# Kernel tuning notes

Hardware: AMD Instinct MI355X
Metric: run time of the kernel (lower is better)

Reference implementation:

```python
import jax, jax.numpy as jnp
import numpy as np

N_NODES = 50000
NEG_SLOPE = 0.2  # PyG GATConv default leaky_relu slope


def setup_inputs() -> dict:
    key = jax.random.key(0)
    ks = jax.random.split(key, 12)
    N, E, D_IN, H = N_NODES, 1200000, 128, 64
    sd_in = 1.0 / np.sqrt(D_IN)
    sd_h = 1.0 / np.sqrt(H)
    return {
        "x": jax.random.normal(ks[0], (N, D_IN), jnp.float32),
        "src": jax.random.randint(ks[1], (E,), 0, N, jnp.int32),
        "dst": jax.random.randint(ks[2], (E,), 0, N, jnp.int32),
        "W1_src": jax.random.normal(ks[3], (D_IN, H), jnp.float32) * sd_in,
        "W1_dst": jax.random.normal(ks[4], (D_IN, H), jnp.float32) * sd_in,
        "a1_src": jax.random.normal(ks[5], (H,), jnp.float32) * sd_h,
        "a1_dst": jax.random.normal(ks[6], (H,), jnp.float32) * sd_h,
        "b1": jnp.zeros((H,), jnp.float32),
        "W2_src": jax.random.normal(ks[7], (H, H), jnp.float32) * sd_h,
        "W2_dst": jax.random.normal(ks[8], (H, H), jnp.float32) * sd_h,
        "a2_src": jax.random.normal(ks[9], (H,), jnp.float32) * sd_h,
        "a2_dst": jax.random.normal(ks[10], (H,), jnp.float32) * sd_h,
        "b2": jnp.zeros((H,), jnp.float32),
    }


def _gat_layer(x, src, dst, W_src, W_dst, att_src, att_dst, bias):
    N = x.shape[0]
    h_src = x @ W_src            # [N, H] transformed source features
    h_dst = x @ W_dst            # [N, H] transformed destination features
    alpha_src = h_src @ att_src  # [N]
    alpha_dst = h_dst @ att_dst  # [N]
    # edge-wise attention logits (gather), edge j -> i: e = lrelu(a_src[j] + a_dst[i])
    e = jax.nn.leaky_relu(alpha_src[src] + alpha_dst[dst], NEG_SLOPE)  # [E]
    # segment softmax over incoming edges of each destination node
    m = jax.ops.segment_max(e, dst, num_segments=N)          # [N]
    ex = jnp.exp(e - m[dst])                                  # [E]
    denom = jax.ops.segment_sum(ex, dst, num_segments=N)     # [N]
    alpha = ex / denom[dst]                                   # [E]
    # weighted scatter-add aggregation
    msgs = h_src[src] * alpha[:, None]                        # [E, H]
    out = jax.ops.segment_sum(msgs, dst, num_segments=N)     # [N, H]
    return out + bias


def reference(x, src, dst, W1_src, W1_dst, a1_src, a1_dst, b1,
              W2_src, W2_dst, a2_src, a2_dst, b2):
    h = jnp.tanh(_gat_layer(x, src, dst, W1_src, W1_dst, a1_src, a1_dst, b1))
    h = jnp.tanh(_gat_layer(h, src, dst, W2_src, W2_dst, a2_src, a2_dst, b2))
    return h
```

## Files before the change

kernel.cpp:

```cpp
#include <hip/hip_runtime.h>
#include <hip/hip_bf16.h>

#define NEG_SLOPE 0.2f
#define EPB 4096

typedef __attribute__((ext_vector_type(8))) short short8v;
typedef __attribute__((ext_vector_type(4))) float f32x4;

__device__ inline float blo(unsigned u) { return __uint_as_float(u << 16); }
__device__ inline float bhi(unsigned u) { return __uint_as_float(u & 0xffff0000u); }
__device__ inline unsigned short bf16bits(float f) {
    __hip_bfloat16 b = __float2bfloat16(f);
    return *(unsigned short*)&b;
}
__device__ inline unsigned pack2bf(float e, float o) {
    return ((unsigned)bf16bits(o) << 16) | (unsigned)bf16bits(e);
}

__global__ void init_counts(int* __restrict__ bucket_cnt) {
    bucket_cnt[threadIdx.x] = 0;
}

__global__ __launch_bounds__(256) void bucket_hist(const int* __restrict__ dst,
                                                   int* __restrict__ bucket_cnt, int E) {
    __shared__ int lh[256];
    int tid = threadIdx.x;
    lh[tid] = 0;
    __syncthreads();
    for (int e = blockIdx.x * 256 + tid; e < E; e += gridDim.x * 256)
        atomicAdd(&lh[dst[e] >> 8], 1);
    __syncthreads();
    if (lh[tid]) atomicAdd(&bucket_cnt[tid], lh[tid]);
}

__global__ __launch_bounds__(256) void bucket_scan(const int* __restrict__ bucket_cnt,
                                                   int* __restrict__ bucket_base,
                                                   int* __restrict__ bucket_cursor, int NB) {
    __shared__ int tmp[256];
    int tid = threadIdx.x;
    int v = (tid < NB) ? bucket_cnt[tid] : 0;
    tmp[tid] = v;
    __syncthreads();
    for (int off = 1; off < 256; off <<= 1) {
        int t = (tid >= off) ? tmp[tid - off] : 0;
        __syncthreads();
        tmp[tid] += t;
        __syncthreads();
    }
    int excl = tmp[tid] - v;
    bucket_base[tid] = excl;
    bucket_cursor[tid] = excl;
    if (tid == 255) bucket_base[256] = tmp[255];
}

__global__ __launch_bounds__(256) void bucket_scatter(const int* __restrict__ src,
                                                      const int* __restrict__ dst,
                                                      int* __restrict__ bucket_cursor,
                                                      unsigned* __restrict__ ebuf, int E) {
    __shared__ int lhist[256];
    __shared__ int lbase[256];
    int tid = threadIdx.x;
    lhist[tid] = 0;
    __syncthreads();
    int base = blockIdx.x * EPB;
    int bkt[16], rank[16];
    unsigned pack[16];
    #pragma unroll
    for (int i = 0; i < 16; ++i) {
        int e = base + i * 256 + tid;
        bkt[i] = -1;
        if (e < E) {
            int d = dst[e], s = src[e];
            bkt[i]  = d >> 8;
            pack[i] = ((unsigned)(d & 255) << 16) | (unsigned)s;
            rank[i] = atomicAdd(&lhist[bkt[i]], 1);
        }
    }
    __syncthreads();
    int cnt = lhist[tid];
    if (cnt) lbase[tid] = atomicAdd(&bucket_cursor[tid], cnt);
    __syncthreads();
    #pragma unroll
    for (int i = 0; i < 16; ++i)
        if (bkt[i] >= 0) ebuf[lbase[bkt[i]] + rank[i]] = pack[i];
}

__global__ __launch_bounds__(256) void bucket_build(const unsigned* __restrict__ ebuf,
                                                    const int* __restrict__ bucket_base,
                                                    int* __restrict__ row_ptr,
                                                    int* __restrict__ csr_src,
                                                    int N, int E) {
    __shared__ int deg[256];
    __shared__ int cur[256];
    __shared__ int tmp[256];
    int b = blockIdx.x, tid = threadIdx.x;
    int ebase = bucket_base[b], eend = bucket_base[b + 1];
    deg[tid] = 0;
    __syncthreads();
    for (int e = ebase + tid; e < eend; e += 256)
        atomicAdd(&deg[ebuf[e] >> 16], 1);
    __syncthreads();
    int v = deg[tid];
    tmp[tid] = v;
    __syncthreads();
    for (int off = 1; off < 256; off <<= 1) {
        int t = (tid >= off) ? tmp[tid - off] : 0;
        __syncthreads();
        tmp[tid] += t;
        __syncthreads();
    }
    int excl = tmp[tid] - v;
    int node = b * 256 + tid;
    if (node < N) row_ptr[node] = ebase + excl;
    if (b == 0 && tid == 0) row_ptr[N] = E;
    cur[tid] = excl;
    __syncthreads();
    for (int e = ebase + tid; e < eend; e += 256) {
        unsigned pk = ebuf[e];
        int r = atomicAdd(&cur[pk >> 16], 1);
        csr_src[ebase + r] = (int)(pk & 0xFFFFu);
    }
}

template <int K>
__global__ __launch_bounds__(256) void node_transform_mfma(
    const float* __restrict__ x,
    const float* __restrict__ W_src,
    const float* __restrict__ a_src,
    const float* __restrict__ W_dst,
    const float* __restrict__ a_dst,
    unsigned* __restrict__ hb_out,
    float* __restrict__ alpha_src,
    float* __restrict__ alpha_dst,
    int N) {
    constexpr int PAD = K + 8;
    __shared__ unsigned short sBt[80 * PAD];

    int tid = threadIdx.x;
    for (int i = tid; i < 64 * K; i += 256) {
        int k = i >> 6, j = i & 63;
        sBt[j * PAD + k] = bf16bits(W_src[i]);
    }
    for (int i = tid; i < 2 * K; i += 256) {
        int which = (i >= K) ? 1 : 0;
        int k = i - which * K;
        const float* Wr = (which ? W_dst : W_src) + k * 64;
        const float* av = which ? a_dst : a_src;
        float s = 0.f;
        #pragma unroll
        for (int j = 0; j < 64; ++j) s += Wr[j] * av[j];
        sBt[(64 + which) * PAD + k] = bf16bits(s);
    }
    for (int i = tid; i < 14 * K; i += 256) {
        int j = 66 + i / K, k = i % K;
        sBt[j * PAD + k] = 0;
    }
    __syncthreads();

    int wid = tid >> 6, l = tid & 63;
    int rowbase = blockIdx.x * 64 + wid * 16;
    int r_load = rowbase + (l & 15);
    if (r_load >= N) r_load = N - 1;
    int kgrp = (l >> 4) * 8;

    f32x4 acc[5];
    #pragma unroll
    for (int t = 0; t < 5; ++t) acc[t] = (f32x4){0.f, 0.f, 0.f, 0.f};

    const float* xr = x + (size_t)r_load * K + kgrp;
    int jcol = l & 15;
    #pragma unroll
    for (int kt = 0; kt < K / 32; ++kt) {
        float4 xa = *(const float4*)(xr + kt * 32);
        float4 xb = *(const float4*)(xr + kt * 32 + 4);
        short8v a;
        a[0] = (short)bf16bits(xa.x); a[1] = (short)bf16bits(xa.y);
        a[2] = (short)bf16bits(xa.z); a[3] = (short)bf16bits(xa.w);
        a[4] = (short)bf16bits(xb.x); a[5] = (short)bf16bits(xb.y);
        a[6] = (short)bf16bits(xb.z); a[7] = (short)bf16bits(xb.w);
        int kbase = kt * 32 + kgrp;
        #pragma unroll
        for (int t = 0; t < 5; ++t) {
            short8v b = *(const short8v*)&sBt[(t * 16 + jcol) * PAD + kbase];
            acc[t] = __builtin_amdgcn_mfma_f32_16x16x32_bf16(a, b, acc[t], 0, 0, 0);
        }
    }

    int rbase = rowbase + (l >> 4) * 4;
    #pragma unroll
    for (int t = 0; t < 4; ++t) {
        #pragma unroll
        for (int r = 0; r < 4; ++r) {
            float v = acc[t][r];
            float w = __shfl_xor(v, 1);
            int row = rbase + r;
            if (!(l & 1) && row < N)
                hb_out[(size_t)row * 32 + t * 8 + (jcol >> 1)] = pack2bf(v, w);
        }
    }
    #pragma unroll
    for (int r = 0; r < 4; ++r) {
        int row = rbase + r;
        if (row < N) {
            if (jcol == 0) alpha_src[row] = acc[4][r];
            if (jcol == 1) alpha_dst[row] = acc[4][r];
        }
    }
}

__global__ __launch_bounds__(256) void aggregate(
    const int* __restrict__ row_ptr, const int* __restrict__ csr_src,
    const float* __restrict__ alpha_src, const float* __restrict__ alpha_dst,
    const unsigned* __restrict__ hb,
    const float* __restrict__ bias,
    float* __restrict__ out,
    int N) {
    int wid = threadIdx.x >> 6, lane = threadIdx.x & 63;
    int node = blockIdx.x * 4 + wid;
    if (node >= N) return;

    int beg = row_ptr[node], end = row_ptr[node + 1];
    float adst = alpha_dst[node];
    int half = lane >> 5, sub = lane & 31;

    float m = -1e30f, denom = 0.f;
    float aA0 = 0.f, aB0 = 0.f, aA1 = 0.f, aB1 = 0.f;
    float aA2 = 0.f, aB2 = 0.f, aA3 = 0.f, aB3 = 0.f;

    for (int c = beg; c < end; c += 64) {
        int cnt = end - c;
        cnt = (cnt < 64) ? cnt : 64;

        int s = 0;
        float el = -1e30f;
        if (lane < cnt) {
            s = csr_src[c + lane];
            float t = alpha_src[s] + adst;
            el = (t > 0.f) ? t : NEG_SLOPE * t;
        }
        float cm = el;
        #pragma unroll
        for (int off = 32; off; off >>= 1) cm = fmaxf(cm, __shfl_xor(cm, off));
        float mn = fmaxf(m, cm);
        float scale = __expf(m - mn);
        float p = (lane < cnt) ? __expf(el - mn) : 0.f;
        float ps = p;
        #pragma unroll
        for (int off = 32; off; off >>= 1) ps += __shfl_xor(ps, off);
        denom = denom * scale + ps;
        aA0 *= scale; aB0 *= scale; aA1 *= scale; aB1 *= scale;
        aA2 *= scale; aB2 *= scale; aA3 *= scale; aB3 *= scale;
        m = mn;

        int j = 0;
        for (; j + 8 <= cnt; j += 8) {
            int e0 = j + half, e1 = j + 2 + half, e2 = j + 4 + half, e3 = j + 6 + half;
            int s0 = __shfl(s, e0), s1 = __shfl(s, e1);
            int s2 = __shfl(s, e2), s3 = __shfl(s, e3);
            float p0 = __shfl(p, e0), p1 = __shfl(p, e1);
            float p2 = __shfl(p, e2), p3 = __shfl(p, e3);
            unsigned u0 = hb[(size_t)s0 * 32 + sub];
            unsigned u1 = hb[(size_t)s1 * 32 + sub];
            unsigned u2 = hb[(size_t)s2 * 32 + sub];
            unsigned u3 = hb[(size_t)s3 * 32 + sub];
            aA0 = fmaf(p0, blo(u0), aA0); aB0 = fmaf(p0, bhi(u0), aB0);
            aA1 = fmaf(p1, blo(u1), aA1); aB1 = fmaf(p1, bhi(u1), aB1);
            aA2 = fmaf(p2, blo(u2), aA2); aB2 = fmaf(p2, bhi(u2), aB2);
            aA3 = fmaf(p3, blo(u3), aA3); aB3 = fmaf(p3, bhi(u3), aB3);
        }
        for (; j < cnt; j += 2) {
            int e = j + half;
            int ec = (e < cnt) ? e : j;
            float pe = __shfl(p, ec);
            if (e >= cnt) pe = 0.f;
            int se = __shfl(s, ec);
            unsigned u = hb[(size_t)se * 32 + sub];
            aA0 = fmaf(pe, blo(u), aA0);
            aB0 = fmaf(pe, bhi(u), aB0);
        }
    }
    float accA = (aA0 + aA1) + (aA2 + aA3);
    float accB = (aB0 + aB1) + (aB2 + aB3);
    accA += __shfl_xor(accA, 32);
    accB += __shfl_xor(accB, 32);
    int srcl = lane >> 1;
    float vA = __shfl(accA, srcl);
    float vB = __shfl(accB, srcl);
    float val = (lane & 1) ? vB : vA;
    float r = (denom > 0.f) ? (val / denom) : 0.f;
    out[(size_t)node * 64 + lane] = tanhf(r + bias[lane]);
}

extern "C" void kernel_launch(void* const* d_in, const int* in_sizes, int n_in,
                              void* d_out, int out_size, void* d_ws, size_t ws_size,
                              hipStream_t stream) {
    const float* x      = (const float*)d_in[0];
    const int*   src    = (const int*)  d_in[1];
    const int*   dst    = (const int*)  d_in[2];
    const float* W1_src = (const float*)d_in[3];
    const float* W1_dst = (const float*)d_in[4];
    const float* a1_src = (const float*)d_in[5];
    const float* a1_dst = (const float*)d_in[6];
    const float* b1     = (const float*)d_in[7];
    const float* W2_src = (const float*)d_in[8];
    const float* W2_dst = (const float*)d_in[9];
    const float* a2_src = (const float*)d_in[10];
    const float* a2_dst = (const float*)d_in[11];
    const float* b2     = (const float*)d_in[12];
    float* out = (float*)d_out;

    const int N = in_sizes[0] / 128;
    const int E = in_sizes[1];
    const int NB = (N + 255) / 256;

    char* ws = (char*)d_ws;
    size_t off = 0;
    auto alloc = [&](size_t bytes) {
        void* p = ws + off;
        off += (bytes + 255) & ~(size_t)255;
        return p;
    };
    unsigned* hbuf   = (unsigned*)alloc((size_t)N * 32 * 4);
    float* bufB      = (float*)alloc((size_t)N * 64 * 4);
    float* alpha_src = (float*)alloc((size_t)N * 4);
    float* alpha_dst = (float*)alloc((size_t)N * 4);
    int*   row_ptr   = (int*)  alloc((size_t)(N + 1) * 4);
    int*   csr_src   = (int*)  alloc((size_t)E * 4);
    int*   bucket_cnt    = (int*)alloc(256 * 4);
    int*   bucket_base   = (int*)alloc(257 * 4);
    int*   bucket_cursor = (int*)alloc(256 * 4);
    unsigned* ebuf = (unsigned*)bufB;
    (void)ws_size;

    const int eb3   = (E + EPB - 1) / EPB;
    const int aggb  = (N + 3) / 4;
    const int mfb   = (N + 63) / 64;

    init_counts<<<1, 256, 0, stream>>>(bucket_cnt);
    bucket_hist<<<256, 256, 0, stream>>>(dst, bucket_cnt, E);
    bucket_scan<<<1, 256, 0, stream>>>(bucket_cnt, bucket_base, bucket_cursor, NB);
    bucket_scatter<<<eb3, 256, 0, stream>>>(src, dst, bucket_cursor, ebuf, E);
    bucket_build<<<NB, 256, 0, stream>>>(ebuf, bucket_base, row_ptr, csr_src, N, E);

    node_transform_mfma<128><<<mfb, 256, 0, stream>>>(x, W1_src, a1_src, W1_dst, a1_dst,
                                                      hbuf, alpha_src, alpha_dst, N);
    aggregate<<<aggb, 256, 0, stream>>>(row_ptr, csr_src, alpha_src, alpha_dst,
                                        hbuf, b1, bufB, N);

    node_transform_mfma<64><<<mfb, 256, 0, stream>>>(bufB, W2_src, a2_src, W2_dst, a2_dst,
                                                     hbuf, alpha_src, alpha_dst, N);
    aggregate<<<aggb, 256, 0, stream>>>(row_ptr, csr_src, alpha_src, alpha_dst,
                                        hbuf, b2, out, N);
}
```

Baseline: 158.2 us.

## Drop online-softmax max tracking and store layer-1 output as bf16

The aggregate kernel no longer keeps a running maximum with rescaling. It exponentiates clamped logits directly, sums the denominator per lane and reduces it once at the end. The tail loop is merged into the 8-wide loop, where lanes past the edge count contribute zero weight. The intermediate layer-1 activations are written as packed bf16 and read straight into the second MFMA transform, which halves that traffic and removes the conversion. The risk is overflow or reduced accuracy if logits are large; the clamp at 60 bounds the exponent.

```diff
diff --git a/kernel.cpp b/kernel.cpp
--- a/kernel.cpp
+++ b/kernel.cpp
@@ -122,9 +122,9 @@
     }
 }
 
-template <int K>
+template <int K, bool INBF16>
 __global__ __launch_bounds__(256) void node_transform_mfma(
-    const float* __restrict__ x,
+    const void* __restrict__ x_,
     const float* __restrict__ W_src,
     const float* __restrict__ a_src,
     const float* __restrict__ W_dst,
@@ -167,17 +167,22 @@
     #pragma unroll
     for (int t = 0; t < 5; ++t) acc[t] = (f32x4){0.f, 0.f, 0.f, 0.f};
 
-    const float* xr = x + (size_t)r_load * K + kgrp;
+    const float* xr32 = (const float*)x_ + (size_t)r_load * K + kgrp;
+    const unsigned short* xr16 = (const unsigned short*)x_ + (size_t)r_load * K + kgrp;
     int jcol = l & 15;
     #pragma unroll
     for (int kt = 0; kt < K / 32; ++kt) {
-        float4 xa = *(const float4*)(xr + kt * 32);
-        float4 xb = *(const float4*)(xr + kt * 32 + 4);
         short8v a;
-        a[0] = (short)bf16bits(xa.x); a[1] = (short)bf16bits(xa.y);
-        a[2] = (short)bf16bits(xa.z); a[3] = (short)bf16bits(xa.w);
-        a[4] = (short)bf16bits(xb.x); a[5] = (short)bf16bits(xb.y);
-        a[6] = (short)bf16bits(xb.z); a[7] = (short)bf16bits(xb.w);
+        if constexpr (INBF16) {
+            a = *(const short8v*)(xr16 + kt * 32);
+        } else {
+            float4 xa = *(const float4*)(xr32 + kt * 32);
+            float4 xb = *(const float4*)(xr32 + kt * 32 + 4);
+            a[0] = (short)bf16bits(xa.x); a[1] = (short)bf16bits(xa.y);
+            a[2] = (short)bf16bits(xa.z); a[3] = (short)bf16bits(xa.w);
+            a[4] = (short)bf16bits(xb.x); a[5] = (short)bf16bits(xb.y);
+            a[6] = (short)bf16bits(xb.z); a[7] = (short)bf16bits(xb.w);
+        }
         int kbase = kt * 32 + kgrp;
         #pragma unroll
         for (int t = 0; t < 5; ++t) {
@@ -208,12 +213,13 @@
     }
 }
 
+template <bool OUTBF16>
 __global__ __launch_bounds__(256) void aggregate(
     const int* __restrict__ row_ptr, const int* __restrict__ csr_src,
     const float* __restrict__ alpha_src, const float* __restrict__ alpha_dst,
     const unsigned* __restrict__ hb,
     const float* __restrict__ bias,
-    float* __restrict__ out,
+    void* __restrict__ out_,
     int N) {
     int wid = threadIdx.x >> 6, lane = threadIdx.x & 63;
     int node = blockIdx.x * 4 + wid;
@@ -223,7 +229,7 @@
     float adst = alpha_dst[node];
     int half = lane >> 5, sub = lane & 31;
 
-    float m = -1e30f, denom = 0.f;
+    float dL = 0.f;
     float aA0 = 0.f, aB0 = 0.f, aA1 = 0.f, aB1 = 0.f;
     float aA2 = 0.f, aB2 = 0.f, aA3 = 0.f, aB3 = 0.f;
 
@@ -232,28 +238,16 @@
         cnt = (cnt < 64) ? cnt : 64;
 
         int s = 0;
-        float el = -1e30f;
+        float p = 0.f;
         if (lane < cnt) {
             s = csr_src[c + lane];
             float t = alpha_src[s] + adst;
-            el = (t > 0.f) ? t : NEG_SLOPE * t;
-        }
-        float cm = el;
-        #pragma unroll
-        for (int off = 32; off; off >>= 1) cm = fmaxf(cm, __shfl_xor(cm, off));
-        float mn = fmaxf(m, cm);
-        float scale = __expf(m - mn);
-        float p = (lane < cnt) ? __expf(el - mn) : 0.f;
-        float ps = p;
-        #pragma unroll
-        for (int off = 32; off; off >>= 1) ps += __shfl_xor(ps, off);
-        denom = denom * scale + ps;
-        aA0 *= scale; aB0 *= scale; aA1 *= scale; aB1 *= scale;
-        aA2 *= scale; aB2 *= scale; aA3 *= scale; aB3 *= scale;
-        m = mn;
-
-        int j = 0;
-        for (; j + 8 <= cnt; j += 8) {
+            t = (t > 0.f) ? t : NEG_SLOPE * t;
+            p = __expf(fminf(t, 60.f));
+            dL += p;
+        }
+
+        for (int j = 0; j < cnt; j += 8) {
             int e0 = j + half, e1 = j + 2 + half, e2 = j + 4 + half, e3 = j + 6 + half;
             int s0 = __shfl(s, e0), s1 = __shfl(s, e1);
             int s2 = __shfl(s, e2), s3 = __shfl(s, e3);
@@ -268,17 +262,11 @@
             aA2 = fmaf(p2, blo(u2), aA2); aB2 = fmaf(p2, bhi(u2), aB2);
             aA3 = fmaf(p3, blo(u3), aA3); aB3 = fmaf(p3, bhi(u3), aB3);
         }
-        for (; j < cnt; j += 2) {
-            int e = j + half;
-            int ec = (e < cnt) ? e : j;
-            float pe = __shfl(p, ec);
-            if (e >= cnt) pe = 0.f;
-            int se = __shfl(s, ec);
-            unsigned u = hb[(size_t)se * 32 + sub];
-            aA0 = fmaf(pe, blo(u), aA0);
-            aB0 = fmaf(pe, bhi(u), aB0);
-        }
-    }
+    }
+    float denom = dL;
+    #pragma unroll
+    for (int off = 32; off; off >>= 1) denom += __shfl_xor(denom, off);
+
     float accA = (aA0 + aA1) + (aA2 + aA3);
     float accB = (aB0 + aB1) + (aB2 + aB3);
     accA += __shfl_xor(accA, 32);
@@ -288,7 +276,15 @@
     float vB = __shfl(accB, srcl);
     float val = (lane & 1) ? vB : vA;
     float r = (denom > 0.f) ? (val / denom) : 0.f;
-    out[(size_t)node * 64 + lane] = tanhf(r + bias[lane]);
+    float fv = tanhf(r + bias[lane]);
+
+    if constexpr (OUTBF16) {
+        float fw = __shfl_xor(fv, 1);
+        if (!(lane & 1))
+            ((unsigned*)out_)[(size_t)node * 32 + (lane >> 1)] = pack2bf(fv, fw);
+    } else {
+        ((float*)out_)[(size_t)node * 64 + lane] = fv;
+    }
 }
 
 extern "C" void kernel_launch(void* const* d_in, const int* in_sizes, int n_in,
@@ -321,7 +317,7 @@
         return p;
     };
     unsigned* hbuf   = (unsigned*)alloc((size_t)N * 32 * 4);
-    float* bufB      = (float*)alloc((size_t)N * 64 * 4);
+    unsigned* h1buf  = (unsigned*)alloc((size_t)N * 32 * 4);
     float* alpha_src = (float*)alloc((size_t)N * 4);
     float* alpha_dst = (float*)alloc((size_t)N * 4);
     int*   row_ptr   = (int*)  alloc((size_t)(N + 1) * 4);
@@ -329,7 +325,7 @@
     int*   bucket_cnt    = (int*)alloc(256 * 4);
     int*   bucket_base   = (int*)alloc(257 * 4);
     int*   bucket_cursor = (int*)alloc(256 * 4);
-    unsigned* ebuf = (unsigned*)bufB;
+    unsigned* ebuf = (unsigned*)alloc((size_t)E * 4);
     (void)ws_size;
 
     const int eb3   = (E + EPB - 1) / EPB;
@@ -342,13 +338,13 @@
     bucket_scatter<<<eb3, 256, 0, stream>>>(src, dst, bucket_cursor, ebuf, E);
     bucket_build<<<NB, 256, 0, stream>>>(ebuf, bucket_base, row_ptr, csr_src, N, E);
 
-    node_transform_mfma<128><<<mfb, 256, 0, stream>>>(x, W1_src, a1_src, W1_dst, a1_dst,
-                                                      hbuf, alpha_src, alpha_dst, N);
-    aggregate<<<aggb, 256, 0, stream>>>(row_ptr, csr_src, alpha_src, alpha_dst,
-                                        hbuf, b1, bufB, N);
-
-    node_transform_mfma<64><<<mfb, 256, 0, stream>>>(bufB, W2_src, a2_src, W2_dst, a2_dst,
-                                                     hbuf, alpha_src, alpha_dst, N);
-    aggregate<<<aggb, 256, 0, stream>>>(row_ptr, csr_src, alpha_src, alpha_dst,
-                                        hbuf, b2, out, N);
-}
+    node_transform_mfma<128, false><<<mfb, 256, 0, stream>>>(
+        x, W1_src, a1_src, W1_dst, a1_dst, hbuf, alpha_src, alpha_dst, N);
+    aggregate<true><<<aggb, 256, 0, stream>>>(row_ptr, csr_src, alpha_src, alpha_dst,
+                                              hbuf, b1, h1buf, N);
+
+    node_transform_mfma<64, true><<<mfb, 256, 0, stream>>>(
+        h1buf, W2_src, a2_src, W2_dst, a2_dst, hbuf, alpha_src, alpha_dst, N);
+    aggregate<false><<<aggb, 256, 0, stream>>>(row_ptr, csr_src, alpha_src, alpha_dst,
+                                               hbuf, b2, out, N);
+}
```

New measurement: 149.6 us. -5.4%, faster.
